# Performance work log

Measured on AMD Instinct MI355X. Metric: run time of the kernel, lower is better.

Reference implementation:

```python
import jax, jax.numpy as jnp
import numpy as np

EMBED = 1024
HEADS = 16
HEAD_DIM = EMBED // HEADS
EPS = 1e-5  # torch LayerNorm default


def setup_inputs() -> dict:
    key = jax.random.key(0)
    ks = jax.random.split(key, 11)
    s = 1.0 / np.sqrt(EMBED)
    def lin(kw, kb):
        W = jax.random.uniform(kw, (EMBED, EMBED), jnp.float32, -s, s)
        b = jax.random.uniform(kb, (EMBED,), jnp.float32, -s, s)
        return W, b
    Wq, bq = lin(ks[0], ks[1])
    Wk, bk = lin(ks[2], ks[3])
    Wv, bv = lin(ks[4], ks[5])
    Wo, bo = lin(ks[6], ks[7])
    x = jax.random.normal(ks[8], (2, 2048, EMBED), jnp.float32)
    gamma = jnp.ones((EMBED,), jnp.float32)
    beta = jnp.zeros((EMBED,), jnp.float32)
    return {"x": x, "Wq": Wq, "bq": bq, "Wk": Wk, "bk": bk,
            "Wv": Wv, "bv": bv, "Wo": Wo, "bo": bo,
            "gamma": gamma, "beta": beta}


def _attn(x, Wq, bq, Wk, bk, Wv, bv, Wo, bo, gamma, beta):
    N, S, _ = x.shape
    # torch Linear: y = x @ W.T + b
    q = (x @ Wq.T + bq).reshape(N, S, HEADS, HEAD_DIM).transpose(0, 2, 1, 3)
    k = (x @ Wk.T + bk).reshape(N, S, HEADS, HEAD_DIM).transpose(0, 2, 1, 3)
    v = (x @ Wv.T + bv).reshape(N, S, HEADS, HEAD_DIM).transpose(0, 2, 1, 3)
    energy = jnp.einsum("bhqd,bhkd->bhqk", q, k) / np.sqrt(HEAD_DIM)
    causal = jnp.tril(jnp.ones((S, S), bool))  # [S,S]
    energy = jnp.where(causal[None, None], energy, -jnp.inf)
    attn = jax.nn.softmax(energy, axis=-1)
    out = jnp.einsum("bhqk,bhkd->bhqd", attn, v)
    out = out.transpose(0, 2, 1, 3).reshape(N, S, EMBED)
    out = out @ Wo.T + bo
    # residual + LayerNorm
    h = out + x
    mu = jnp.mean(h, axis=-1, keepdims=True)
    var = jnp.var(h, axis=-1, keepdims=True)
    return (h - mu) * jax.lax.rsqrt(var + EPS) * gamma + beta


def reference(x, Wq, bq, Wk, bk, Wv, bv, Wo, bo, gamma, beta):
    return _attn(x, Wq, bq, Wk, bk, Wv, bv, Wo, bo, gamma, beta)
```

## Files before the change

### kernel.cpp

```cpp
#include <hip/hip_runtime.h>

typedef __attribute__((ext_vector_type(8))) short short8;
typedef __attribute__((ext_vector_type(4))) float f32x4;
typedef __attribute__((ext_vector_type(4))) short short4v;

template<bool B> struct BoolC { static constexpr bool value = B; };

__device__ __forceinline__ short f2bs(float f) {
    union { float f; unsigned u; } c; c.f = f;
    unsigned r = 0x7FFFu + ((c.u >> 16) & 1u);
    return (short)((c.u + r) >> 16);
}

__device__ __forceinline__ unsigned fbits(float f) {
    union { float f; unsigned u; } c; c.f = f; return c.u;
}

__device__ __forceinline__ void gld_lds16(const void* g, void* l) {
    __builtin_amdgcn_global_load_lds(
        (const __attribute__((address_space(1))) unsigned int*)g,
        (__attribute__((address_space(3))) unsigned int*)l, 16, 0, 0);
}

__device__ __forceinline__ f32x4 mfma16(short8 a, short8 b, f32x4 c) {
    return __builtin_amdgcn_mfma_f32_16x16x32_bf16(a, b, c, 0, 0, 0);
}

template<int N> __device__ __forceinline__ void vmwait() {
    if constexpr (N == 0)      asm volatile("s_waitcnt vmcnt(0)" ::: "memory");
    else if constexpr (N == 3) asm volatile("s_waitcnt vmcnt(3)" ::: "memory");
    else if constexpr (N == 4) asm volatile("s_waitcnt vmcnt(4)" ::: "memory");
}

__global__ __launch_bounds__(256) void cvtall_kernel(
    const float* __restrict__ x,
    const float* __restrict__ Wq, const float* __restrict__ Wk,
    const float* __restrict__ Wv, const float* __restrict__ Wo,
    short* __restrict__ xb, short* __restrict__ wqkv, short* __restrict__ wob)
{
    int i = blockIdx.x * 256 + threadIdx.x;
    const float* src; short* dst; int off;
    if (i < 1048576) { src = x; dst = xb; off = i; }
    else {
        int j = i - 1048576, which = j >> 18;
        off = j & 262143;
        src = which == 0 ? Wq : (which == 1 ? Wk : (which == 2 ? Wv : Wo));
        dst = which == 3 ? wob : (wqkv + (size_t)which * 1048576);
    }
    float4 v = ((const float4*)src)[off];
    short4v o;
    o.x = f2bs(v.x); o.y = f2bs(v.y); o.z = f2bs(v.z); o.w = f2bs(v.w);
    ((short4v*)dst)[off] = o;
}

#define BN 128
#define BK 32

template<int MODE, int BMt>
__global__ __launch_bounds__(256) void gemm_bt(
    const short* __restrict__ A, const short* __restrict__ B,
    int M, int N, int K,
    const float* __restrict__ b0, const float* __restrict__ b1, const float* __restrict__ b2,
    short* __restrict__ oq, short* __restrict__ ok_, short* __restrict__ ov,
    const float* __restrict__ bo, const float* __restrict__ xres,
    float* __restrict__ outf)
{
    constexpr int IM = BMt / 32;
    constexpr int BUFSZ = (BMt + BN) * BK;
    constexpr int LPS = (BMt == 128) ? 4 : 3;
    __shared__ __align__(16) short SM[3 * BUFSZ];
    const int tid = threadIdx.x;
    const int wave = tid >> 6, lane = tid & 63;
    const int lhi = lane >> 4, llo = lane & 15;
    const int row0 = blockIdx.x * BMt, col0 = blockIdx.y * BN;
    const int wr = (wave >> 1) * (BMt / 2), wc = (wave & 1) * 64;

    f32x4 acc[IM][4] = {};

    const short* gA0 = A + (size_t)(row0 + (tid >> 2)) * K + (tid & 3) * 8;
    const short* gA1 = A + (size_t)(row0 + 64 + (tid >> 2)) * K + (tid & 3) * 8;
    const short* gB0 = B + (size_t)(col0 + (tid >> 2)) * K + (tid & 3) * 8;
    const short* gB1 = B + (size_t)(col0 + 64 + (tid >> 2)) * K + (tid & 3) * 8;

    auto stage = [&](int kk, int bf) {
        short* As = SM + bf * BUFSZ;
        short* Bs = As + BMt * BK;
        gld_lds16(gA0 + kk, &As[wave * 512]);
        if constexpr (BMt == 128) gld_lds16(gA1 + kk, &As[2048 + wave * 512]);
        gld_lds16(gB0 + kk, &Bs[wave * 512]);
        gld_lds16(gB1 + kk, &Bs[2048 + wave * 512]);
    };

    const int NT = K / BK;
    stage(0, 0);
    stage(BK, 1);

    for (int kt = 0; kt < NT; ++kt) {
        if (kt < NT - 1) vmwait<LPS>(); else vmwait<0>();
        __builtin_amdgcn_s_barrier();
        __builtin_amdgcn_sched_barrier(0);
        if (kt + 2 < NT) {
            int b2i = kt + 2; b2i -= (b2i >= 3) ? 3 : 0; b2i -= (b2i >= 3) ? 3 : 0;
            stage((kt + 2) * BK, (kt + 2) % 3);
        }
        const short* As = SM + (kt % 3) * BUFSZ;
        const short* Bs = As + BMt * BK;
        short8 af[IM], bfr[4];
        #pragma unroll
        for (int i = 0; i < IM; ++i)
            af[i] = *(const short8*)&As[(wr + i * 16 + llo) * BK + lhi * 8];
        #pragma unroll
        for (int j = 0; j < 4; ++j)
            bfr[j] = *(const short8*)&Bs[(wc + j * 16 + llo) * BK + lhi * 8];
        #pragma unroll
        for (int i = 0; i < IM; ++i)
            #pragma unroll
            for (int j = 0; j < 4; ++j)
                acc[i][j] = mfma16(af[i], bfr[j], acc[i][j]);
    }

    if constexpr (MODE == 0) {
        const int which = (int)blockIdx.y >> 3;
        if (which < 2) {
            const float* bia = which == 0 ? b0 : b1;
            short* dst = which == 0 ? oq : ok_;
            #pragma unroll
            for (int i = 0; i < IM; ++i)
                #pragma unroll
                for (int j = 0; j < 4; ++j)
                    #pragma unroll
                    for (int r = 0; r < 4; ++r) {
                        int m = row0 + wr + i * 16 + lhi * 4 + r;
                        int nn = (col0 & 1023) + wc + j * 16 + llo;
                        float v = acc[i][j][r] + bia[nn];
                        int h = nn >> 6, d = nn & 63;
                        int bb = m >> 11, s = m & 2047;
                        dst[((size_t)((bb * 16 + h) * 2048 + s)) * 64 + d] = f2bs(v);
                    }
        } else {
            __syncthreads();
            short* T = SM + wave * (64 * 26);
            const int nn0 = (col0 - 2048) + wc;
            const int h = nn0 >> 6;
            const int bb = row0 >> 11;
            const int s0 = (row0 & 2047) + wr;
            short* vdst = ov + ((size_t)(bb * 16 + h) * 64) * 2048;
            #pragma unroll
            for (int i = 0; i < IM; ++i) {
                #pragma unroll
                for (int j = 0; j < 4; ++j) {
                    const float bias = b2[nn0 + j * 16 + llo];
                    unsigned u01 = __builtin_amdgcn_perm(fbits(acc[i][j][1] + bias),
                                                         fbits(acc[i][j][0] + bias), 0x07060302u);
                    unsigned u23 = __builtin_amdgcn_perm(fbits(acc[i][j][3] + bias),
                                                         fbits(acc[i][j][2] + bias), 0x07060302u);
                    unsigned* Tw = (unsigned*)&T[(j * 16 + llo) * 26];
                    Tw[lhi * 2]     = u01;
                    Tw[lhi * 2 + 1] = u23;
                }
                short8 a0 = *(const short8*)&T[lane * 26];
                short8 a1 = *(const short8*)&T[lane * 26 + 8];
                *(short8*)&vdst[(size_t)lane * 2048 + s0 + i * 16]     = a0;
                *(short8*)&vdst[(size_t)lane * 2048 + s0 + i * 16 + 8] = a1;
            }
        }
    } else {
        #pragma unroll
        for (int i = 0; i < IM; ++i)
            #pragma unroll
            for (int j = 0; j < 4; ++j)
                #pragma unroll
                for (int r = 0; r < 4; ++r) {
                    int m = row0 + wr + i * 16 + lhi * 4 + r;
                    int n = col0 + wc + j * 16 + llo;
                    size_t idx = (size_t)m * N + n;
                    outf[idx] = acc[i][j][r] + bo[n] + xres[idx];
                }
    }
}

#define SCL 0.18033688011f

__global__ __launch_bounds__(256) void attn_kernel(
    const short* __restrict__ Q, const short* __restrict__ K,
    const short* __restrict__ Vt, short* __restrict__ O)
{
    const int id = blockIdx.x;
    const int u = id >> 3;
    const int bh = (id & 7) * 4 + (u & 3);
    const int s4 = u >> 2;
    const int p = (s4 < 8) ? (2 * s4) : (31 - 2 * s4);
    const int q0L = p * 64, q0H = (31 - p) * 64;
    const int ntH = 32 - p;

    const short* Qb = Q  + (size_t)bh * 2048 * 64;
    const short* Kb = K  + (size_t)bh * 2048 * 64;
    const short* Vb = Vt + (size_t)bh * 64 * 2048;

    __shared__ __align__(16) short Ks[2][64 * 64];
    __shared__ __align__(16) short Vs[2][64 * 64];
    __shared__ __align__(16) short Ps[4][2][16 * 68];

    const int tid = threadIdx.x, wave = tid >> 6, lane = tid & 63;
    const int lhi = lane >> 4, llo = lane & 15;
    const int qwL = q0L + wave * 16, qwH = q0H + wave * 16;
    const int qgL = qwL + llo, qgH = qwH + llo;

    auto scale8 = [](short8 a) {
        short8 r;
        #pragma unroll
        for (int i = 0; i < 8; ++i) {
            union { unsigned u; float f; } c; c.u = ((unsigned)(unsigned short)a[i]) << 16;
            r[i] = f2bs(c.f * SCL);
        }
        return r;
    };
    const short8 qfL0 = scale8(*(const short8*)&Qb[(size_t)(qwL + llo) * 64 + lhi * 8]);
    const short8 qfL1 = scale8(*(const short8*)&Qb[(size_t)(qwL + llo) * 64 + 32 + lhi * 8]);
    const short8 qfH0 = scale8(*(const short8*)&Qb[(size_t)(qwH + llo) * 64 + lhi * 8]);
    const short8 qfH1 = scale8(*(const short8*)&Qb[(size_t)(qwH + llo) * 64 + 32 + lhi * 8]);

    const int tr = tid >> 3, tc = tid & 7, sc = tc ^ (tr & 7);
    const short* kS0 = Kb + (size_t)tr * 64 + sc * 8;
    const short* kS1 = Kb + (size_t)(32 + tr) * 64 + sc * 8;
    const short* vS0 = Vb + (size_t)tr * 2048 + sc * 8;
    const short* vS1 = Vb + (size_t)(32 + tr) * 2048 + sc * 8;
    const int dOff = wave * 512;

    f32x4 oL[4] = {}, oH[4] = {};
    float lL = 0.f, lH = 0.f;

    unsigned* PwH = (unsigned*)Ps[wave][0] + llo * 34;
    unsigned* PwL = (unsigned*)Ps[wave][1] + llo * 34;

    gld_lds16(kS0, Ks[0] + dOff);
    gld_lds16(kS1, Ks[0] + 2048 + dOff);
    gld_lds16(vS0, Vs[0] + dOff);
    gld_lds16(vS1, Vs[0] + 2048 + dOff);
    __syncthreads();

    const int swq = (llo & 7) << 3;

    auto smx = [&](f32x4 (&st)[4], float& lrow, unsigned* Pw, int qg, int kk0, bool diag) {
        if (diag) {
            #pragma unroll
            for (int t = 0; t < 4; ++t)
                #pragma unroll
                for (int j = 0; j < 4; ++j)
                    if (kk0 + t * 16 + lhi * 4 + j > qg) st[t][j] = -1e30f;
        }
        float rs0 = 0.f, rs1 = 0.f;
        #pragma unroll
        for (int t = 0; t < 4; ++t) {
            st[t][0] = exp2f(st[t][0]);
            st[t][1] = exp2f(st[t][1]);
            st[t][2] = exp2f(st[t][2]);
            st[t][3] = exp2f(st[t][3]);
            rs0 += st[t][0] + st[t][2];
            rs1 += st[t][1] + st[t][3];
        }
        lrow += rs0 + rs1;
        #pragma unroll
        for (int t = 0; t < 4; ++t) {
            Pw[t * 8 + lhi * 2]     = __builtin_amdgcn_perm(fbits(st[t][1]), fbits(st[t][0]), 0x07060302u);
            Pw[t * 8 + lhi * 2 + 1] = __builtin_amdgcn_perm(fbits(st[t][3]), fbits(st[t][2]), 0x07060302u);
        }
    };

    int cur = 0;
    auto tile = [&](int kt, auto dualc) {
        constexpr bool DUAL = decltype(dualc)::value;
        const int kk0 = kt * 64;
        if (kt + 1 < ntH) {
            const int nk = kk0 + 64;
            gld_lds16(kS0 + (size_t)nk * 64, Ks[cur ^ 1] + dOff);
            gld_lds16(kS1 + (size_t)nk * 64, Ks[cur ^ 1] + 2048 + dOff);
            gld_lds16(vS0 + nk, Vs[cur ^ 1] + dOff);
            gld_lds16(vS1 + nk, Vs[cur ^ 1] + 2048 + dOff);
        }

        f32x4 stH[4], stL[4];
        __builtin_amdgcn_s_setprio(1);
        #pragma unroll
        for (int t = 0; t < 4; ++t) {
            const int row = t * 16 + llo;
            short8 kf0 = *(const short8*)&Ks[cur][row * 64 + ((lhi * 8) ^ swq)];
            short8 kf1 = *(const short8*)&Ks[cur][row * 64 + ((lhi * 8 + 32) ^ swq)];
            f32x4 a = {};
            a = mfma16(kf0, qfH0, a);
            stH[t] = mfma16(kf1, qfH1, a);
            if (DUAL) {
                f32x4 b = {};
                b = mfma16(kf0, qfL0, b);
                stL[t] = mfma16(kf1, qfL1, b);
            }
        }
        __builtin_amdgcn_s_setprio(0);

        smx(stH, lH, PwH, qgH, kk0, kt == ntH - 1);
        if (DUAL) smx(stL, lL, PwL, qgL, kk0, kt == p);

        const short8 pH0 = *(const short8*)&Ps[wave][0][llo * 68 + lhi * 8];
        const short8 pH1 = *(const short8*)&Ps[wave][0][llo * 68 + 32 + lhi * 8];
        short8 pL0, pL1;
        if (DUAL) {
            pL0 = *(const short8*)&Ps[wave][1][llo * 68 + lhi * 8];
            pL1 = *(const short8*)&Ps[wave][1][llo * 68 + 32 + lhi * 8];
        }
        __builtin_amdgcn_s_setprio(1);
        #pragma unroll
        for (int dt = 0; dt < 4; ++dt) {
            const int row = dt * 16 + llo;
            short8 vf0 = *(const short8*)&Vs[cur][row * 64 + ((lhi * 8) ^ swq)];
            short8 vf1 = *(const short8*)&Vs[cur][row * 64 + ((lhi * 8 + 32) ^ swq)];
            oH[dt] = mfma16(pH0, vf0, oH[dt]);
            oH[dt] = mfma16(pH1, vf1, oH[dt]);
            if (DUAL) {
                oL[dt] = mfma16(pL0, vf0, oL[dt]);
                oL[dt] = mfma16(pL1, vf1, oL[dt]);
            }
        }
        __builtin_amdgcn_s_setprio(0);

        if (kt + 1 < ntH) __syncthreads();
        cur ^= 1;
    };

    for (int kt = 0; kt <= p; ++kt)      tile(kt, BoolC<true>{});
    for (int kt = p + 1; kt < ntH; ++kt) tile(kt, BoolC<false>{});

    lH += __shfl_xor(lH, 16); lH += __shfl_xor(lH, 32);
    lL += __shfl_xor(lL, 16); lL += __shfl_xor(lL, 32);
    const int b = bh >> 4, h = bh & 15;
    const float invH = 1.f / lH, invL = 1.f / lL;
    #pragma unroll
    for (int j = 0; j < 4; ++j) {
        const float ivH = __shfl(invH, lhi * 4 + j);
        const float ivL = __shfl(invL, lhi * 4 + j);
        const size_t rowH = (size_t)(b * 2048 + qwH + lhi * 4 + j);
        const size_t rowL = (size_t)(b * 2048 + qwL + lhi * 4 + j);
        #pragma unroll
        for (int dt = 0; dt < 4; ++dt) {
            int d = dt * 16 + llo;
            O[rowH * 1024 + h * 64 + d] = f2bs(oH[dt][j] * ivH);
            O[rowL * 1024 + h * 64 + d] = f2bs(oL[dt][j] * ivL);
        }
    }
}

__global__ __launch_bounds__(256) void ln_kernel(float* __restrict__ out,
        const float* __restrict__ gamma, const float* __restrict__ beta)
{
    const int row = blockIdx.x;
    float* p = out + (size_t)row * 1024;
    const int tid = threadIdx.x;
    float4 v = ((const float4*)p)[tid];
    float s = v.x + v.y + v.z + v.w;
    float ss = v.x * v.x + v.y * v.y + v.z * v.z + v.w * v.w;
    #pragma unroll
    for (int d = 1; d < 64; d <<= 1) {
        s  += __shfl_xor(s, d);
        ss += __shfl_xor(ss, d);
    }
    __shared__ float red[8];
    const int wave = tid >> 6, lane = tid & 63;
    if (lane == 0) { red[wave] = s; red[4 + wave] = ss; }
    __syncthreads();
    s  = red[0] + red[1] + red[2] + red[3];
    ss = red[4] + red[5] + red[6] + red[7];
    const float mu = s * (1.0f / 1024.0f);
    const float var = ss * (1.0f / 1024.0f) - mu * mu;
    const float rstd = rsqrtf(var + 1e-5f);
    float4 g = ((const float4*)gamma)[tid];
    float4 b = ((const float4*)beta)[tid];
    v.x = (v.x - mu) * rstd * g.x + b.x;
    v.y = (v.y - mu) * rstd * g.y + b.y;
    v.z = (v.z - mu) * rstd * g.z + b.z;
    v.w = (v.w - mu) * rstd * g.w + b.w;
    ((float4*)p)[tid] = v;
}

extern "C" void kernel_launch(void* const* d_in, const int* in_sizes, int n_in,
                              void* d_out, int out_size, void* d_ws, size_t ws_size,
                              hipStream_t stream)
{
    const float* x  = (const float*)d_in[0];
    const float* Wq = (const float*)d_in[1];
    const float* bq = (const float*)d_in[2];
    const float* Wk = (const float*)d_in[3];
    const float* bk = (const float*)d_in[4];
    const float* Wv = (const float*)d_in[5];
    const float* bv = (const float*)d_in[6];
    const float* Wo = (const float*)d_in[7];
    const float* bo = (const float*)d_in[8];
    const float* gamma = (const float*)d_in[9];
    const float* beta  = (const float*)d_in[10];
    float* out = (float*)d_out;

    char* ws = (char*)d_ws;
    short* xb   = (short*)(ws);
    short* wqkv = (short*)(ws + (8ull  << 20));
    short* wob  = (short*)(ws + (14ull << 20));
    short* qb   = (short*)(ws + (16ull << 20));
    short* kb   = (short*)(ws + (24ull << 20));
    short* vtb  = (short*)(ws + (32ull << 20));
    short* ab   = xb;

    cvtall_kernel<<<8192, 256, 0, stream>>>(x, Wq, Wk, Wv, Wo, xb, wqkv, wob);

    gemm_bt<0, 128><<<dim3(32, 24), 256, 0, stream>>>(xb, wqkv, 4096, 3072, 1024,
        bq, bk, bv, qb, kb, vtb, nullptr, nullptr, nullptr);

    attn_kernel<<<512, 256, 0, stream>>>(qb, kb, vtb, ab);

    gemm_bt<1, 64><<<dim3(64, 8), 256, 0, stream>>>(ab, wob, 4096, 1024, 1024,
        nullptr, nullptr, nullptr, nullptr, nullptr, nullptr, bo, x, out);

    ln_kernel<<<4096, 256, 0, stream>>>(out, gamma, beta);
}
```

Measured before the change: 117.5 us.

## Triple-buffer K/V tiles in attention kernel with prefetch distance two

```diff
diff --git a/kernel.cpp b/kernel.cpp
--- a/kernel.cpp
+++ b/kernel.cpp
@@ -99,10 +99,7 @@
         if (kt < NT - 1) vmwait<LPS>(); else vmwait<0>();
         __builtin_amdgcn_s_barrier();
         __builtin_amdgcn_sched_barrier(0);
-        if (kt + 2 < NT) {
-            int b2i = kt + 2; b2i -= (b2i >= 3) ? 3 : 0; b2i -= (b2i >= 3) ? 3 : 0;
-            stage((kt + 2) * BK, (kt + 2) % 3);
-        }
+        if (kt + 2 < NT) stage((kt + 2) * BK, (kt + 2) % 3);
         const short* As = SM + (kt % 3) * BUFSZ;
         const short* Bs = As + BMt * BK;
         short8 af[IM], bfr[4];
@@ -197,8 +194,8 @@
     const short* Kb = K  + (size_t)bh * 2048 * 64;
     const short* Vb = Vt + (size_t)bh * 64 * 2048;
 
-    __shared__ __align__(16) short Ks[2][64 * 64];
-    __shared__ __align__(16) short Vs[2][64 * 64];
+    __shared__ __align__(16) short Ks[3][64 * 64];
+    __shared__ __align__(16) short Vs[3][64 * 64];
     __shared__ __align__(16) short Ps[4][2][16 * 68];
 
     const int tid = threadIdx.x, wave = tid >> 6, lane = tid & 63;
@@ -233,11 +230,17 @@
     unsigned* PwH = (unsigned*)Ps[wave][0] + llo * 34;
     unsigned* PwL = (unsigned*)Ps[wave][1] + llo * 34;
 
-    gld_lds16(kS0, Ks[0] + dOff);
-    gld_lds16(kS1, Ks[0] + 2048 + dOff);
-    gld_lds16(vS0, Vs[0] + dOff);
-    gld_lds16(vS1, Vs[0] + 2048 + dOff);
-    __syncthreads();
+    auto stageKV = [&](int kt) {
+        const int bf3 = kt % 3;
+        const int nk = kt * 64;
+        gld_lds16(kS0 + (size_t)nk * 64, Ks[bf3] + dOff);
+        gld_lds16(kS1 + (size_t)nk * 64, Ks[bf3] + 2048 + dOff);
+        gld_lds16(vS0 + nk, Vs[bf3] + dOff);
+        gld_lds16(vS1 + nk, Vs[bf3] + 2048 + dOff);
+    };
+
+    stageKV(0);
+    stageKV(1);
 
     const int swq = (llo & 7) << 3;
 
@@ -267,25 +270,22 @@
         }
     };
 
-    int cur = 0;
     auto tile = [&](int kt, auto dualc) {
         constexpr bool DUAL = decltype(dualc)::value;
         const int kk0 = kt * 64;
-        if (kt + 1 < ntH) {
-            const int nk = kk0 + 64;
-            gld_lds16(kS0 + (size_t)nk * 64, Ks[cur ^ 1] + dOff);
-            gld_lds16(kS1 + (size_t)nk * 64, Ks[cur ^ 1] + 2048 + dOff);
-            gld_lds16(vS0 + nk, Vs[cur ^ 1] + dOff);
-            gld_lds16(vS1 + nk, Vs[cur ^ 1] + 2048 + dOff);
-        }
+        if (kt < ntH - 1) vmwait<4>(); else vmwait<0>();
+        __builtin_amdgcn_s_barrier();
+        __builtin_amdgcn_sched_barrier(0);
+        if (kt + 2 < ntH) stageKV(kt + 2);
+        const int bf3 = kt % 3;
 
         f32x4 stH[4], stL[4];
         __builtin_amdgcn_s_setprio(1);
         #pragma unroll
         for (int t = 0; t < 4; ++t) {
             const int row = t * 16 + llo;
-            short8 kf0 = *(const short8*)&Ks[cur][row * 64 + ((lhi * 8) ^ swq)];
-            short8 kf1 = *(const short8*)&Ks[cur][row * 64 + ((lhi * 8 + 32) ^ swq)];
+            short8 kf0 = *(const short8*)&Ks[bf3][row * 64 + ((lhi * 8) ^ swq)];
+            short8 kf1 = *(const short8*)&Ks[bf3][row * 64 + ((lhi * 8 + 32) ^ swq)];
             f32x4 a = {};
             a = mfma16(kf0, qfH0, a);
             stH[t] = mfma16(kf1, qfH1, a);
@@ -311,8 +311,8 @@
         #pragma unroll
         for (int dt = 0; dt < 4; ++dt) {
             const int row = dt * 16 + llo;
-            short8 vf0 = *(const short8*)&Vs[cur][row * 64 + ((lhi * 8) ^ swq)];
-            short8 vf1 = *(const short8*)&Vs[cur][row * 64 + ((lhi * 8 + 32) ^ swq)];
+            short8 vf0 = *(const short8*)&Vs[bf3][row * 64 + ((lhi * 8) ^ swq)];
+            short8 vf1 = *(const short8*)&Vs[bf3][row * 64 + ((lhi * 8 + 32) ^ swq)];
             oH[dt] = mfma16(pH0, vf0, oH[dt]);
             oH[dt] = mfma16(pH1, vf1, oH[dt]);
             if (DUAL) {
@@ -321,9 +321,6 @@
             }
         }
         __builtin_amdgcn_s_setprio(0);
-
-        if (kt + 1 < ntH) __syncthreads();
-        cur ^= 1;
     };
 
     for (int kt = 0; kt <= p; ++kt)      tile(kt, BoolC<true>{});
```

Result: no change. 119.3 us (+1.5%).

## Switch GEMM to double buffering with XCD-aware block swizzle and occupancy hint

Applied to the files above, without the earlier changes.

```diff
diff --git a/kernel.cpp b/kernel.cpp
--- a/kernel.cpp
+++ b/kernel.cpp
@@ -24,12 +24,6 @@
 
 __device__ __forceinline__ f32x4 mfma16(short8 a, short8 b, f32x4 c) {
     return __builtin_amdgcn_mfma_f32_16x16x32_bf16(a, b, c, 0, 0, 0);
-}
-
-template<int N> __device__ __forceinline__ void vmwait() {
-    if constexpr (N == 0)      asm volatile("s_waitcnt vmcnt(0)" ::: "memory");
-    else if constexpr (N == 3) asm volatile("s_waitcnt vmcnt(3)" ::: "memory");
-    else if constexpr (N == 4) asm volatile("s_waitcnt vmcnt(4)" ::: "memory");
 }
 
 __global__ __launch_bounds__(256) void cvtall_kernel(
@@ -57,7 +51,7 @@
 #define BK 32
 
 template<int MODE, int BMt>
-__global__ __launch_bounds__(256) void gemm_bt(
+__global__ __launch_bounds__(256, 5) void gemm_bt(
     const short* __restrict__ A, const short* __restrict__ B,
     int M, int N, int K,
     const float* __restrict__ b0, const float* __restrict__ b1, const float* __restrict__ b2,
@@ -67,12 +61,16 @@
 {
     constexpr int IM = BMt / 32;
     constexpr int BUFSZ = (BMt + BN) * BK;
-    constexpr int LPS = (BMt == 128) ? 4 : 3;
-    __shared__ __align__(16) short SM[3 * BUFSZ];
+    __shared__ __align__(16) short SM[2 * BUFSZ];
     const int tid = threadIdx.x;
     const int wave = tid >> 6, lane = tid & 63;
     const int lhi = lane >> 4, llo = lane & 15;
-    const int row0 = blockIdx.x * BMt, col0 = blockIdx.y * BN;
+
+    const int nwg = gridDim.x, chunk = nwg >> 3;
+    const int f = blockIdx.x;
+    const int swz = (f & 7) * chunk + (f >> 3);
+    const int nx = M / BMt;
+    const int row0 = (swz % nx) * BMt, col0 = (swz / nx) * BN;
     const int wr = (wave >> 1) * (BMt / 2), wc = (wave & 1) * 64;
 
     f32x4 acc[IM][4] = {};
@@ -93,17 +91,13 @@
 
     const int NT = K / BK;
     stage(0, 0);
-    stage(BK, 1);
 
     for (int kt = 0; kt < NT; ++kt) {
-        if (kt < NT - 1) vmwait<LPS>(); else vmwait<0>();
+        asm volatile("s_waitcnt vmcnt(0)" ::: "memory");
         __builtin_amdgcn_s_barrier();
         __builtin_amdgcn_sched_barrier(0);
-        if (kt + 2 < NT) {
-            int b2i = kt + 2; b2i -= (b2i >= 3) ? 3 : 0; b2i -= (b2i >= 3) ? 3 : 0;
-            stage((kt + 2) * BK, (kt + 2) % 3);
-        }
-        const short* As = SM + (kt % 3) * BUFSZ;
+        if (kt + 1 < NT) stage((kt + 1) * BK, (kt + 1) & 1);
+        const short* As = SM + (kt & 1) * BUFSZ;
         const short* Bs = As + BMt * BK;
         short8 af[IM], bfr[4];
         #pragma unroll
@@ -120,7 +114,7 @@
     }
 
     if constexpr (MODE == 0) {
-        const int which = (int)blockIdx.y >> 3;
+        const int which = (col0 >> 10);
         if (which < 2) {
             const float* bia = which == 0 ? b0 : b1;
             short* dst = which == 0 ? oq : ok_;
@@ -408,12 +402,12 @@
 
     cvtall_kernel<<<8192, 256, 0, stream>>>(x, Wq, Wk, Wv, Wo, xb, wqkv, wob);
 
-    gemm_bt<0, 128><<<dim3(32, 24), 256, 0, stream>>>(xb, wqkv, 4096, 3072, 1024,
+    gemm_bt<0, 128><<<768, 256, 0, stream>>>(xb, wqkv, 4096, 3072, 1024,
         bq, bk, bv, qb, kb, vtb, nullptr, nullptr, nullptr);
 
     attn_kernel<<<512, 256, 0, stream>>>(qb, kb, vtb, ab);
 
-    gemm_bt<1, 64><<<dim3(64, 8), 256, 0, stream>>>(ab, wob, 4096, 1024, 1024,
+    gemm_bt<1, 64><<<512, 256, 0, stream>>>(ab, wob, 4096, 1024, 1024,
         nullptr, nullptr, nullptr, nullptr, nullptr, nullptr, bo, x, out);
 
     ln_kernel<<<4096, 256, 0, stream>>>(out, gamma, beta);
```

Result: slower. 120.0 us (+2.1%).
